# Kernel tuning notes

Hardware: AMD Instinct MI355X
Metric: run time of the kernel (lower is better)

The kernel has to match this reference:

```python
import jax, jax.numpy as jnp
import numpy as np

N = 50000
E = 800000
R = 8
F_IN = 128
H = 128          # num_hidden
F_OUT = 128      # num_outputs
D1, D2, D3 = 2 * H, H, F_OUT


def _glorot(key, shape):
    fan_in, fan_out = shape[-2], shape[-1]
    lim = np.sqrt(6.0 / (fan_in + fan_out)).astype(np.float32)
    return jax.random.uniform(key, shape, jnp.float32, -lim, lim)


def setup_inputs() -> dict:
    key = jax.random.key(0)
    ks = jax.random.split(key, 12)
    x = jax.random.normal(ks[0], (N, F_IN), jnp.float32)
    edge_index = jax.random.randint(ks[1], (2, E), 0, N, jnp.int64)
    edge_type = jax.random.randint(ks[2], (E,), 0, R, jnp.int64)
    return {
        "x": x,
        "edge_index": edge_index,
        "edge_type": edge_type,
        "w1": _glorot(ks[3], (R, F_IN, D1)),
        "root1": _glorot(ks[4], (F_IN, D1)),
        "b1": jnp.zeros((D1,), jnp.float32),
        "w2": _glorot(ks[5], (R, D1, D2)),
        "root2": _glorot(ks[6], (D1, D2)),
        "b2": jnp.zeros((D2,), jnp.float32),
        "w3": _glorot(ks[7], (R, D2, D3)),
        "root3": _glorot(ks[8], (D2, D3)),
        "b3": jnp.zeros((D3,), jnp.float32),
    }


def _rgcn_layer(h, src, dst, seg, inv_cnt, W, root, bias):
    # Per-relation mean aggregation via a fused (dst, rel) segment id,
    # then a grouped contraction with the per-relation weights.
    n, fin = h.shape
    s = jax.ops.segment_sum(h[src], seg, num_segments=n * R)  # [N*R, fin]
    agg = s.reshape(n, R, fin) * inv_cnt                      # mean per (node, rel)
    return jnp.einsum("nri,rio->no", agg, W) + h @ root + bias


def reference(x, edge_index, edge_type, w1, root1, b1, w2, root2, b2, w3, root3, b3):
    src, dst = edge_index[0], edge_index[1]
    seg = dst * R + edge_type                                  # fused (dst, rel) id
    cnt = jax.ops.segment_sum(jnp.ones((E,), x.dtype), seg, num_segments=N * R)
    inv_cnt = (1.0 / jnp.maximum(cnt, 1.0)).reshape(N, R, 1)

    h1 = jax.nn.elu(_rgcn_layer(x, src, dst, seg, inv_cnt, w1, root1, b1))
    # dropout: identity (eval mode)
    h2 = jax.nn.elu(_rgcn_layer(h1, src, dst, seg, inv_cnt, w2, root2, b2))
    h3 = jax.nn.elu(_rgcn_layer(h2, src, dst, seg, inv_cnt, w3, root3, b3))
    return jnp.concatenate([h1, h2, h3], axis=1)               # [N, D1+D2+D3]
```

## Files before the change

kernel.cpp:

```cpp
#include <hip/hip_runtime.h>


#define DEVI __device__ __forceinline__

constexpr int NN    = 50000;
constexpr int EE    = 800000;
constexpr int RREL  = 8;
constexpr int NRSEG = NN * RREL;
constexpr int NTC   = 1152;
constexpr int MT1   = (NN + 127) / 128;

using u16 = unsigned short;
using u32 = unsigned int;
using u64 = unsigned long long;

typedef short short8 __attribute__((ext_vector_type(8)));
typedef float f32x4  __attribute__((ext_vector_type(4)));

DEVI float bf2f(u32 u){ union{u32 i; float f;} x; x.i = u << 16; return x.f; }
DEVI u16   f2b(float f){ u32 u = __float_as_uint(f); u32 r = u + 0x7fffu + ((u >> 16) & 1u); return (u16)(r >> 16); }

typedef const __attribute__((address_space(1))) u32 gas_u32;
typedef __attribute__((address_space(3))) u32       las_u32;
DEVI void gload16(const void* g, void* l){
  __builtin_amdgcn_global_load_lds((gas_u32*)(u64)g, (las_u32*)(u64)l, 16, 0, 0);
}


__global__ void count_k(const int* __restrict__ dst, const int* __restrict__ et, int* __restrict__ cnt){
  int e = blockIdx.x * 256 + threadIdx.x;
  if(e < EE) atomicAdd(&cnt[dst[e] * RREL + et[e]], 1);
}

constexpr int SCAN_E = 8;
constexpr int CHUNK  = 2048;
constexpr int NB     = (NRSEG + CHUNK - 1) / CHUNK;

__global__ void scan1_k(const int* __restrict__ cnt, int* __restrict__ bsums){
  __shared__ int sm[256];
  int b = blockIdx.x, t = threadIdx.x;
  int base = b * CHUNK + t * SCAN_E;
  int s = 0;
  #pragma unroll
  for(int j = 0; j < SCAN_E; j++){ int i = base + j; s += (i < NRSEG) ? cnt[i] : 0; }
  sm[t] = s; __syncthreads();
  for(int off = 128; off > 0; off >>= 1){ if(t < off) sm[t] += sm[t + off]; __syncthreads(); }
  if(t == 0) bsums[b] = sm[0];
}

__global__ void scan2_k(int* __restrict__ bsums){
  __shared__ int sm[256];
  int t = threadIdx.x;
  int v = (t < NB) ? bsums[t] : 0;
  sm[t] = v; __syncthreads();
  for(int off = 1; off < 256; off <<= 1){
    int x = (t >= off) ? sm[t - off] : 0; __syncthreads();
    sm[t] += x; __syncthreads();
  }
  if(t < NB) bsums[t] = sm[t] - v;
}

__global__ void scan3i_k(const int* __restrict__ cnt, const int* __restrict__ bsums,
                         int* __restrict__ offs, float* __restrict__ inv){
  __shared__ int sm[256];
  int b = blockIdx.x, t = threadIdx.x;
  int base = b * CHUNK + t * SCAN_E;
  int loc[SCAN_E]; int cv[SCAN_E]; int run = 0;
  #pragma unroll
  for(int j = 0; j < SCAN_E; j++){
    int i = base + j; int c = (i < NRSEG) ? cnt[i] : 0;
    cv[j] = c; loc[j] = run; run += c;
  }
  sm[t] = run; __syncthreads();
  for(int off = 1; off < 256; off <<= 1){
    int x = (t >= off) ? sm[t - off] : 0; __syncthreads();
    sm[t] += x; __syncthreads();
  }
  int tb = bsums[b] + sm[t] - run;
  #pragma unroll
  for(int j = 0; j < SCAN_E; j++){
    int i = base + j;
    if(i < NRSEG){
      offs[i] = tb + loc[j];
      inv[i]  = 1.0f / (float)(cv[j] > 0 ? cv[j] : 1);
    }
  }
  if(b == 0 && t == 0) offs[NRSEG] = EE;
}

__global__ void fill_k(const int* __restrict__ src, const int* __restrict__ dst, const int* __restrict__ et,
                       const int* __restrict__ offs, int* __restrict__ fill, int* __restrict__ spk){
  int e = blockIdx.x * 256 + threadIdx.x;
  if(e < EE){
    int d = dst[e], r = et[e];
    int seg = d * RREL + r;
    int i = atomicAdd(&fill[seg], 1);
    spk[offs[seg] + i] = (src[e] << 3) | r;
  }
}

constexpr int PR0 = NN * 128;
constexpr int PR1 = 256 * NTC;
constexpr int PR2 = 9 * 256 * 128;
constexpr int PR3 = 9 * 128 * 128;
constexpr int PRT = PR0 + PR1 + PR2 + PR3;

__global__ void prep_pack_k(const float* __restrict__ x, u16* __restrict__ xb, u16* __restrict__ agg2,
                            const float* __restrict__ w1, const float* __restrict__ root1, u16* __restrict__ wpL1,
                            const float* __restrict__ w2, const float* __restrict__ root2, u16* __restrict__ wp2,
                            const float* __restrict__ w3, const float* __restrict__ root3, u16* __restrict__ wp3){
  int idx = blockIdx.x * 256 + threadIdx.x;
  if(idx < PR0){
    u16 v = f2b(x[idx]);
    xb[idx] = v;
    int n = idx >> 7, c = idx & 127;
    agg2[(size_t)n * NTC + 1024 + c] = v;
    return;
  }
  idx -= PR0;
  if(idx < PR1){
    int o = idx / NTC, k = idx % NTC;
    int g = k >> 7, i = k & 127;
    float v = (g < RREL) ? w1[((size_t)g * 128 + i) * 256 + o] : root1[(size_t)i * 256 + o];
    wpL1[idx] = f2b(v);
    return;
  }
  idx -= PR1;
  if(idx < PR2){
    int i = idx % 256;
    int o = (idx / 256) % 128;
    int g = idx / (256 * 128);
    float v = (g < RREL) ? w2[((size_t)g * 256 + i) * 128 + o] : root2[(size_t)i * 128 + o];
    wp2[idx] = f2b(v);
    return;
  }
  idx -= PR2;
  if(idx < PR3){
    int i = idx % 128;
    int o = (idx / 128) % 128;
    int g = idx / (128 * 128);
    float v = (g < RREL) ? w3[((size_t)g * 128 + i) * 128 + o] : root3[(size_t)i * 128 + o];
    wp3[idx] = f2b(v);
  }
}


DEVI void acc8(float* a, uint4 v){
  a[0] += bf2f(v.x & 0xffffu); a[1] += bf2f(v.x >> 16);
  a[2] += bf2f(v.y & 0xffffu); a[3] += bf2f(v.y >> 16);
  a[4] += bf2f(v.z & 0xffffu); a[5] += bf2f(v.z >> 16);
  a[6] += bf2f(v.w & 0xffffu); a[7] += bf2f(v.w >> 16);
}

DEVI void fma8(float* a, uint4 v, float c){
  a[0] += c * bf2f(v.x & 0xffffu); a[1] += c * bf2f(v.x >> 16);
  a[2] += c * bf2f(v.y & 0xffffu); a[3] += c * bf2f(v.y >> 16);
  a[4] += c * bf2f(v.z & 0xffffu); a[5] += c * bf2f(v.z >> 16);
  a[6] += c * bf2f(v.w & 0xffffu); a[7] += c * bf2f(v.w >> 16);
}

template<int FIN, int RSUB, int LDW>
__global__ __launch_bounds__(256)
void agg_k(const u16* __restrict__ hb, const int* __restrict__ spk,
           const int* __restrict__ offs, const float* __restrict__ inv,
           u16* __restrict__ agg, int r0)
{
  constexpr int G = FIN / 8;
  const int gl  = threadIdx.x & (G - 1);
  int gid = (int)((blockIdx.x * blockDim.x + threadIdx.x) / G);
  const int ng = (int)((gridDim.x * blockDim.x) / G);
  const int S = NN * RSUB;
  for(int s = gid; s < S; s += ng){
    int n = s / RSUB, rr = s - n * RSUB;
    int seg = n * RREL + r0 + rr;
    int beg = offs[seg], end = offs[seg + 1];
    float sc = inv[seg];
    float acc[8];
    #pragma unroll
    for(int i = 0; i < 8; i++) acc[i] = 0.f;
    int e = beg;
    for(; e + 2 <= end; e += 2){
      int s0 = spk[e] >> 3, s1 = spk[e + 1] >> 3;
      uint4 v0 = ((const uint4*)(hb + (size_t)s0 * FIN))[gl];
      uint4 v1 = ((const uint4*)(hb + (size_t)s1 * FIN))[gl];
      acc8(acc, v0);
      acc8(acc, v1);
    }
    if(e < end){
      uint4 v0 = ((const uint4*)(hb + (size_t)(spk[e] >> 3) * FIN))[gl];
      acc8(acc, v0);
    }
    uint4 o;
    o.x = (u32)f2b(acc[0] * sc) | ((u32)f2b(acc[1] * sc) << 16);
    o.y = (u32)f2b(acc[2] * sc) | ((u32)f2b(acc[3] * sc) << 16);
    o.z = (u32)f2b(acc[4] * sc) | ((u32)f2b(acc[5] * sc) << 16);
    o.w = (u32)f2b(acc[6] * sc) | ((u32)f2b(acc[7] * sc) << 16);
    ((uint4*)(agg + (size_t)n * LDW + rr * FIN))[gl] = o;
  }
}


template<int K, int NJC, int EPI, int SWZ>
__global__ __launch_bounds__(512)
void dgemm_k(const u16* __restrict__ A, const u16* __restrict__ Bw,
             u16* __restrict__ T, const float* __restrict__ bias,
             float* __restrict__ dout, u16* __restrict__ hbout)
{
  constexpr int NKS = K / 32;
  constexpr int ASL = 512;
  constexpr int BSL = 512;
  constexpr int LPS = 2;
  __shared__ u16 lds[3][(ASL + BSL) * 8];
  int bm, jc;
  if constexpr(SWZ == 1){
    int d = (int)blockIdx.x;
    int x = d & 7, s = d >> 3;
    jc = s & 1;
    bm = x + 8 * (s >> 1);
    if(bm >= MT1) return;
  } else {
    bm = (int)blockIdx.x / NJC;
    jc = (int)blockIdx.x % NJC;
  }
  const int tid = threadIdx.x;
  const int wid = tid >> 6, lane = tid & 63;
  const int wm  = wid >> 1, wn = wid & 1;

  auto stage = [&](int ks, u16* l){
    u16* lA = l;
    u16* lB = l + ASL * 8;
    int koff = ks * 32;
    {
      int sb = wid * 64;
      int s  = sb + lane;
      int pair = s >> 3, cs = s & 7;
      int c    = cs ^ (pair & 7);
      int row  = pair * 2 + (c >> 2);
      int k8   = c & 3;
      int kk   = koff + k8 * 8;
      int rowg = bm * 128 + row; rowg = rowg < NN ? rowg : NN - 1;
      gload16(A + (size_t)rowg * K + kk, lA + sb * 8);
    }
    {
      int sb = wid * 64;
      int s  = sb + lane;
      int pair = s >> 3, cs = s & 7;
      int c    = cs ^ (pair & 7);
      int row  = pair * 2 + (c >> 2);
      int k8   = c & 3;
      int kk   = koff + k8 * 8;
      gload16(Bw + ((size_t)(jc * 128 + row)) * K + kk, lB + sb * 8);
    }
  };

  auto ldfrag = [&](const u16* buf, int row, int k8){
    int pair = row >> 1;
    int c    = ((row & 1) << 2) + k8;
    int cs   = c ^ (pair & 7);
    return *(const short8*)(buf + pair * 64 + cs * 8);
  };

  f32x4 acc[2][4] = {};

  stage(0, (u16*)lds[0]);
  stage(1, (u16*)lds[1]);
  for(int ks = 0; ks < NKS; ks++){
    if(ks + 1 < NKS){
      asm volatile("s_waitcnt vmcnt(%0)" :: "i"(LPS) : "memory");
    } else {
      asm volatile("s_waitcnt vmcnt(0)" ::: "memory");
    }
    __builtin_amdgcn_sched_barrier(0);
    __builtin_amdgcn_s_barrier();
    __builtin_amdgcn_sched_barrier(0);
    if(ks + 2 < NKS) stage(ks + 2, (u16*)lds[(ks + 2) % 3]);
    const u16* lA = (const u16*)lds[ks % 3];
    const u16* lB = lA + ASL * 8;
    short8 af[2], bf4[4];
    #pragma unroll
    for(int m = 0; m < 2; m++) af[m] = ldfrag(lA, wm * 32 + m * 16 + (lane & 15), lane >> 4);
    #pragma unroll
    for(int n = 0; n < 4; n++) bf4[n] = ldfrag(lB, wn * 64 + n * 16 + (lane & 15), lane >> 4);
    #pragma unroll
    for(int m = 0; m < 2; m++)
      #pragma unroll
      for(int n = 0; n < 4; n++)
        acc[m][n] = __builtin_amdgcn_mfma_f32_16x16x32_bf16(af[m], bf4[n], acc[m][n], 0, 0, 0);
  }

  #pragma unroll
  for(int m = 0; m < 2; m++){
    #pragma unroll
    for(int j = 0; j < 4; j++){
      int grow = bm * 128 + wm * 32 + m * 16 + (lane >> 4) * 4 + j;
      if(grow >= NN) continue;
      #pragma unroll
      for(int n = 0; n < 4; n++){
        int lcol = wn * 64 + n * 16 + (lane & 15);
        if constexpr(EPI == 0){
          T[(size_t)grow * NTC + jc * 128 + lcol] = f2b(acc[m][n][j]);
        } else {
          int gcol = jc * 128 + lcol;
          float v = acc[m][n][j] + bias[gcol];
          v = v > 0.f ? v : expm1f(v);
          dout[(size_t)grow * 512 + gcol] = v;
          hbout[(size_t)grow * 256 + gcol] = f2b(v);
        }
      }
    }
  }
}


template<bool HB>
__global__ __launch_bounds__(256)
void scat_k(const u16* __restrict__ T, const int* __restrict__ spk,
            const int* __restrict__ offs, const float* __restrict__ inv,
            const float* __restrict__ bias, float* __restrict__ dout, int dcol0,
            u16* __restrict__ hbout)
{
  const int gl = threadIdx.x & 15;
  int n = (int)((blockIdx.x * 256 + threadIdx.x) >> 4);
  if(n >= NN) return;
  const float* invn = inv + n * RREL;
  float acc[8];
  {
    uint4 v = *(const uint4*)(T + (size_t)n * NTC + 1024 + gl * 8);
    acc[0] = bf2f(v.x & 0xffffu); acc[1] = bf2f(v.x >> 16);
    acc[2] = bf2f(v.y & 0xffffu); acc[3] = bf2f(v.y >> 16);
    acc[4] = bf2f(v.z & 0xffffu); acc[5] = bf2f(v.z >> 16);
    acc[6] = bf2f(v.w & 0xffffu); acc[7] = bf2f(v.w >> 16);
  }
  int e  = offs[n * RREL];
  int e1 = offs[n * RREL + RREL];
  for(; e + 8 <= e1; e += 8){
    int p[8];
    #pragma unroll
    for(int j = 0; j < 8; j++) p[j] = spk[e + j];
    uint4 v[8];
    #pragma unroll
    for(int j = 0; j < 8; j++)
      v[j] = *(const uint4*)(T + (size_t)(p[j] >> 3) * NTC + (p[j] & 7) * 128 + gl * 8);
    #pragma unroll
    for(int j = 0; j < 8; j++) fma8(acc, v[j], invn[p[j] & 7]);
  }
  for(; e + 4 <= e1; e += 4){
    int p0 = spk[e], p1 = spk[e + 1], p2 = spk[e + 2], p3 = spk[e + 3];
    uint4 v0 = *(const uint4*)(T + (size_t)(p0 >> 3) * NTC + (p0 & 7) * 128 + gl * 8);
    uint4 v1 = *(const uint4*)(T + (size_t)(p1 >> 3) * NTC + (p1 & 7) * 128 + gl * 8);
    uint4 v2 = *(const uint4*)(T + (size_t)(p2 >> 3) * NTC + (p2 & 7) * 128 + gl * 8);
    uint4 v3 = *(const uint4*)(T + (size_t)(p3 >> 3) * NTC + (p3 & 7) * 128 + gl * 8);
    fma8(acc, v0, invn[p0 & 7]); fma8(acc, v1, invn[p1 & 7]);
    fma8(acc, v2, invn[p2 & 7]); fma8(acc, v3, invn[p3 & 7]);
  }
  for(; e < e1; e++){
    int p0 = spk[e];
    uint4 v0 = *(const uint4*)(T + (size_t)(p0 >> 3) * NTC + (p0 & 7) * 128 + gl * 8);
    fma8(acc, v0, invn[p0 & 7]);
  }
  float o[8];
  #pragma unroll
  for(int i = 0; i < 8; i++){
    float v = acc[i] + bias[gl * 8 + i];
    o[i] = v > 0.f ? v : expm1f(v);
  }
  float4* dp = (float4*)(dout + (size_t)n * 512 + dcol0 + gl * 8);
  dp[0] = make_float4(o[0], o[1], o[2], o[3]);
  dp[1] = make_float4(o[4], o[5], o[6], o[7]);
  if(HB){
    uint4 hv;
    hv.x = (u32)f2b(o[0]) | ((u32)f2b(o[1]) << 16);
    hv.y = (u32)f2b(o[2]) | ((u32)f2b(o[3]) << 16);
    hv.z = (u32)f2b(o[4]) | ((u32)f2b(o[5]) << 16);
    hv.w = (u32)f2b(o[6]) | ((u32)f2b(o[7]) << 16);
    *(uint4*)(hbout + (size_t)n * 128 + gl * 8) = hv;
  }
}


extern "C" void kernel_launch(void* const* d_in, const int* in_sizes, int n_in,
                              void* d_out, int out_size, void* d_ws, size_t ws_size,
                              hipStream_t stream)
{
  const float* x     = (const float*)d_in[0];
  const int*   ei    = (const int*)d_in[1];
  const int*   et    = (const int*)d_in[2];
  const float* w1    = (const float*)d_in[3];
  const float* root1 = (const float*)d_in[4];
  const float* b1    = (const float*)d_in[5];
  const float* w2    = (const float*)d_in[6];
  const float* root2 = (const float*)d_in[7];
  const float* b2    = (const float*)d_in[8];
  const float* w3    = (const float*)d_in[9];
  const float* root3 = (const float*)d_in[10];
  const float* b3    = (const float*)d_in[11];
  float* out = (float*)d_out;

  const int* esrc = ei;
  const int* edst = ei + EE;

  char* w = (char*)d_ws;
  auto alloc = [&](size_t bytes)->char*{ char* p = w; w += (bytes + 255) & ~(size_t)255; return p; };
  int*   cnt   = (int*)  alloc((size_t)NRSEG * 4);
  int*   offs  = (int*)  alloc((size_t)(NRSEG + 1) * 4);
  int*   fill  = (int*)  alloc((size_t)NRSEG * 4);
  float* inv   = (float*)alloc((size_t)NRSEG * 4);
  int*   spk   = (int*)  alloc((size_t)EE * 4);
  u16*   xb    = (u16*)  alloc((size_t)NN * 128 * 2);
  u16*   h1b   = (u16*)  alloc((size_t)NN * 256 * 2);
  u16*   h2b   = (u16*)  alloc((size_t)NN * 128 * 2);
  u16*   wpL1  = (u16*)  alloc((size_t)256 * NTC * 2);
  u16*   wp2   = (u16*)  alloc((size_t)9 * 256 * 128 * 2);
  u16*   wp3   = (u16*)  alloc((size_t)9 * 128 * 128 * 2);
  int*   bsums = (int*)  alloc(1024 * 4);
  u16*   agg2  = (u16*)  alloc((size_t)NN * NTC * 2);
  u16*   T     = (u16*)  alloc((size_t)NN * NTC * 2);
  (void)ws_size; (void)in_sizes; (void)n_in; (void)out_size;

  hipMemsetAsync(cnt,  0, (size_t)NRSEG * 4, stream);
  hipMemsetAsync(fill, 0, (size_t)NRSEG * 4, stream);

  count_k<<<(EE + 255) / 256, 256, 0, stream>>>(edst, et, cnt);
  scan1_k<<<NB, 256, 0, stream>>>(cnt, bsums);
  scan2_k<<<1, 256, 0, stream>>>(bsums);
  scan3i_k<<<NB, 256, 0, stream>>>(cnt, bsums, offs, inv);
  fill_k<<<(EE + 255) / 256, 256, 0, stream>>>(esrc, edst, et, offs, fill, spk);
  prep_pack_k<<<(PRT + 255) / 256, 256, 0, stream>>>(
      x, xb, agg2, w1, root1, wpL1, w2, root2, wp2, w3, root3, wp3);

  const int MT = (NN + 127) / 128;
  const int SB = (NN * 16 + 255) / 256;

  agg_k<128, 8, NTC><<<4096, 256, 0, stream>>>(xb, spk, offs, inv, agg2, 0);
  dgemm_k<NTC, 2, 1, 1><<<784, 512, 0, stream>>>(agg2, wpL1, nullptr, b1, out, h1b);

  dgemm_k<256, 9, 0, 0><<<MT * 9, 512, 0, stream>>>(h1b, wp2, T, nullptr, nullptr, nullptr);
  scat_k<true><<<SB, 256, 0, stream>>>(T, spk, offs, inv, b2, out, 256, h2b);

  dgemm_k<128, 9, 0, 0><<<MT * 9, 512, 0, stream>>>(h2b, wp3, T, nullptr, nullptr, nullptr);
  scat_k<false><<<SB, 256, 0, stream>>>(T, spk, offs, inv, b3, out, 384, nullptr);
}
```

Measured before the change: 423.1 us.

## Read root input directly from xb in layer-1 GEMM and deepen its pipeline

Layer 1 no longer copies the bf16 input x into the root columns of the aggregated buffer. The GEMM now loads those last K-slices straight from xb, and the aggregated buffer shrinks from 1152 to 1024 columns. This removes a strided scatter write in the prep kernel and some buffer footprint. Separately, the layer-1 GEMM gets a 4-deep LDS multi-buffer pipeline with adjusted vmcnt waits, while layers 2 and 3 keep depth 3. This uses more LDS per block, which may lower occupancy.

```diff
diff --git a/kernel.cpp b/kernel.cpp
--- a/kernel.cpp
+++ b/kernel.cpp
@@ -105,16 +105,13 @@
 constexpr int PR3 = 9 * 128 * 128;
 constexpr int PRT = PR0 + PR1 + PR2 + PR3;
 
-__global__ void prep_pack_k(const float* __restrict__ x, u16* __restrict__ xb, u16* __restrict__ agg2,
+__global__ void prep_pack_k(const float* __restrict__ x, u16* __restrict__ xb,
                             const float* __restrict__ w1, const float* __restrict__ root1, u16* __restrict__ wpL1,
                             const float* __restrict__ w2, const float* __restrict__ root2, u16* __restrict__ wp2,
                             const float* __restrict__ w3, const float* __restrict__ root3, u16* __restrict__ wp3){
   int idx = blockIdx.x * 256 + threadIdx.x;
   if(idx < PR0){
-    u16 v = f2b(x[idx]);
-    xb[idx] = v;
-    int n = idx >> 7, c = idx & 127;
-    agg2[(size_t)n * NTC + 1024 + c] = v;
+    xb[idx] = f2b(x[idx]);
     return;
   }
   idx -= PR0;
@@ -200,17 +197,18 @@
 }
 
 
-template<int K, int NJC, int EPI, int SWZ>
+template<int K, int NJC, int EPI, int SWZ, int DEPTH, bool XROOT>
 __global__ __launch_bounds__(512)
 void dgemm_k(const u16* __restrict__ A, const u16* __restrict__ Bw,
              u16* __restrict__ T, const float* __restrict__ bias,
-             float* __restrict__ dout, u16* __restrict__ hbout)
+             float* __restrict__ dout, u16* __restrict__ hbout,
+             const u16* __restrict__ Ax)
 {
   constexpr int NKS = K / 32;
+  constexpr int KA  = XROOT ? 1024 : K;
   constexpr int ASL = 512;
   constexpr int BSL = 512;
-  constexpr int LPS = 2;
-  __shared__ u16 lds[3][(ASL + BSL) * 8];
+  __shared__ u16 lds[DEPTH][(ASL + BSL) * 8];
   int bm, jc;
   if constexpr(SWZ == 1){
     int d = (int)blockIdx.x;
@@ -239,7 +237,14 @@
       int k8   = c & 3;
       int kk   = koff + k8 * 8;
       int rowg = bm * 128 + row; rowg = rowg < NN ? rowg : NN - 1;
-      gload16(A + (size_t)rowg * K + kk, lA + sb * 8);
+      const u16* ga;
+      if constexpr(XROOT){
+        ga = (koff >= 1024) ? (Ax + (size_t)rowg * 128 + (kk - 1024))
+                            : (A  + (size_t)rowg * KA  + kk);
+      } else {
+        ga = A + (size_t)rowg * KA + kk;
+      }
+      gload16(ga, lA + sb * 8);
     }
     {
       int sb = wid * 64;
@@ -262,19 +267,21 @@
 
   f32x4 acc[2][4] = {};
 
-  stage(0, (u16*)lds[0]);
-  stage(1, (u16*)lds[1]);
+  #pragma unroll
+  for(int p = 0; p < DEPTH - 1; p++) stage(p, (u16*)lds[p]);
   for(int ks = 0; ks < NKS; ks++){
-    if(ks + 1 < NKS){
-      asm volatile("s_waitcnt vmcnt(%0)" :: "i"(LPS) : "memory");
+    if(ks <= NKS - DEPTH + 1){
+      asm volatile("s_waitcnt vmcnt(%0)" :: "i"(2 * (DEPTH - 2)) : "memory");
+    } else if(DEPTH == 4 && ks == NKS - 2){
+      asm volatile("s_waitcnt vmcnt(2)" ::: "memory");
     } else {
       asm volatile("s_waitcnt vmcnt(0)" ::: "memory");
     }
     __builtin_amdgcn_sched_barrier(0);
     __builtin_amdgcn_s_barrier();
     __builtin_amdgcn_sched_barrier(0);
-    if(ks + 2 < NKS) stage(ks + 2, (u16*)lds[(ks + 2) % 3]);
-    const u16* lA = (const u16*)lds[ks % 3];
+    if(ks + DEPTH - 1 < NKS) stage(ks + DEPTH - 1, (u16*)lds[(ks + DEPTH - 1) % DEPTH]);
+    const u16* lA = (const u16*)lds[ks % DEPTH];
     const u16* lB = lA + ASL * 8;
     short8 af[2], bf4[4];
     #pragma unroll
@@ -413,7 +420,7 @@
   u16*   wp2   = (u16*)  alloc((size_t)9 * 256 * 128 * 2);
   u16*   wp3   = (u16*)  alloc((size_t)9 * 128 * 128 * 2);
   int*   bsums = (int*)  alloc(1024 * 4);
-  u16*   agg2  = (u16*)  alloc((size_t)NN * NTC * 2);
+  u16*   agg2  = (u16*)  alloc((size_t)NN * 1024 * 2);
   u16*   T     = (u16*)  alloc((size_t)NN * NTC * 2);
   (void)ws_size; (void)in_sizes; (void)n_in; (void)out_size;
 
@@ -426,17 +433,20 @@
   scan3i_k<<<NB, 256, 0, stream>>>(cnt, bsums, offs, inv);
   fill_k<<<(EE + 255) / 256, 256, 0, stream>>>(esrc, edst, et, offs, fill, spk);
   prep_pack_k<<<(PRT + 255) / 256, 256, 0, stream>>>(
-      x, xb, agg2, w1, root1, wpL1, w2, root2, wp2, w3, root3, wp3);
+      x, xb, w1, root1, wpL1, w2, root2, wp2, w3, root3, wp3);
 
   const int MT = (NN + 127) / 128;
   const int SB = (NN * 16 + 255) / 256;
 
-  agg_k<128, 8, NTC><<<4096, 256, 0, stream>>>(xb, spk, offs, inv, agg2, 0);
-  dgemm_k<NTC, 2, 1, 1><<<784, 512, 0, stream>>>(agg2, wpL1, nullptr, b1, out, h1b);
-
-  dgemm_k<256, 9, 0, 0><<<MT * 9, 512, 0, stream>>>(h1b, wp2, T, nullptr, nullptr, nullptr);
+  agg_k<128, 8, 1024><<<4096, 256, 0, stream>>>(xb, spk, offs, inv, agg2, 0);
+  dgemm_k<NTC, 2, 1, 1, 4, true><<<784, 512, 0, stream>>>(
+      agg2, wpL1, nullptr, b1, out, h1b, xb);
+
+  dgemm_k<256, 9, 0, 0, 3, false><<<MT * 9, 512, 0, stream>>>(
+      h1b, wp2, T, nullptr, nullptr, nullptr, nullptr);
   scat_k<true><<<SB, 256, 0, stream>>>(T, spk, offs, inv, b2, out, 256, h2b);
 
-  dgemm_k<128, 9, 0, 0><<<MT * 9, 512, 0, stream>>>(h2b, wp3, T, nullptr, nullptr, nullptr);
+  dgemm_k<128, 9, 0, 0, 3, false><<<MT * 9, 512, 0, stream>>>(
+      h2b, wp3, T, nullptr, nullptr, nullptr, nullptr);
   scat_k<false><<<SB, 256, 0, stream>>>(T, spk, offs, inv, b3, out, 384, nullptr);
 }
```

Result: faster. 411.0 us (-2.9%).
